# Kernel optimization log

Hardware: AMD Instinct MI355X
Metric: run time of the kernel (lower is better)

The kernel has to match this reference:

```python
import jax, jax.numpy as jnp
import numpy as np
import math

WH, WW = 8, 8
N = WH * WW            # tokens per window = 64
DIM = 128
H = 4                  # num_heads
HD = DIM // H          # head_dim = 32
B_ = 3072              # num_windows * batch
NW = 192               # windows per image (96/8 * 128/8)
LAMBDA_INIT = 0.8 - 0.6 * math.exp(-0.3 * 0)  # layer_idx = 0 -> 0.2
EPS_RMS = 1e-9


def _polar_input():
    # Polar-coordinate relative positions, as in __init__
    gy, gx = jnp.meshgrid(jnp.arange(WH), jnp.arange(WW), indexing='ij')
    flat = jnp.stack([gy.reshape(-1), gx.reshape(-1)])          # (2, N)
    rel = flat[:, :, None] - flat[:, None, :]                   # (2, N, N)
    dx = rel[1].astype(jnp.float32)
    dy = -rel[0].astype(jnp.float32)
    r = jnp.sqrt(dx * dx + dy * dy + 1e-9)
    theta = jnp.arctan2(dx, dy)
    max_r = math.sqrt((WH - 1) ** 2 + (WW - 1) ** 2)
    return jnp.stack([r / max_r, (theta + math.pi) / (2 * math.pi)], axis=-1)  # (N, N, 2)


def setup_inputs() -> dict:
    key = jax.random.key(0)
    ks = jax.random.split(key, 16)
    s = 0.02
    inp = {}
    inp['x'] = jax.random.normal(ks[0], (B_, N, DIM), jnp.float32)
    inp['mask'] = jnp.zeros((NW, N, N), jnp.float32)
    inp['Wqkv'] = jax.random.normal(ks[1], (3 * DIM, DIM), jnp.float32) * s
    inp['bqkv'] = jnp.zeros((3 * DIM,), jnp.float32)
    inp['Wqkv2'] = jax.random.normal(ks[2], (2 * DIM, DIM), jnp.float32) * s
    inp['bqkv2'] = jnp.zeros((2 * DIM,), jnp.float32)
    inp['Wp1'] = jax.random.normal(ks[3], (64, 2), jnp.float32) * 0.1
    inp['bp1'] = jnp.zeros((64,), jnp.float32)
    inp['Wp2'] = jax.random.normal(ks[4], (H, 64), jnp.float32) * 0.1
    inp['bp2'] = jnp.zeros((H,), jnp.float32)
    inp['lambda_q1'] = jax.random.normal(ks[5], (HD // 2,), jnp.float32) * 0.1
    inp['lambda_k1'] = jax.random.normal(ks[6], (HD // 2,), jnp.float32) * 0.1
    inp['lambda_q2'] = jax.random.normal(ks[7], (HD // 2,), jnp.float32) * 0.1
    inp['lambda_k2'] = jax.random.normal(ks[8], (HD // 2,), jnp.float32) * 0.1
    inp['subln_w'] = jnp.ones((HD,), jnp.float32)
    inp['Wproj'] = jax.random.normal(ks[9], (DIM, DIM), jnp.float32) * s
    inp['bproj'] = jnp.zeros((DIM,), jnp.float32)
    return inp


def reference(x, mask, Wqkv, bqkv, Wqkv2, bqkv2, Wp1, bp1, Wp2, bp2,
              lambda_q1, lambda_k1, lambda_q2, lambda_k2, subln_w, Wproj, bproj):
    scale = HD ** -0.5
    # primary q, k, v
    qkv = (x @ Wqkv.T + bqkv).reshape(B_, N, 3, H, HD).transpose(2, 0, 3, 1, 4)
    q, k, v = qkv[0] * scale, qkv[1], qkv[2]        # (B_, H, N, HD)
    # secondary q2, k2 for differential attention
    qk2 = (x @ Wqkv2.T + bqkv2).reshape(B_, N, 2, H, HD).transpose(2, 0, 3, 1, 4)
    q2, k2 = qk2[0] * scale, qk2[1]

    attn = jnp.einsum('bhnd,bhmd->bhnm', q, k)      # (B_, H, N, N)
    attn2 = jnp.einsum('bhnd,bhmd->bhnm', q2, k2)

    lam = (jnp.exp(jnp.sum(lambda_q1 * lambda_k1))
           - jnp.exp(jnp.sum(lambda_q2 * lambda_k2)) + LAMBDA_INIT)

    # MLP-based polar relative position bias (exact erf GELU, as nn.GELU)
    pin = _polar_input().reshape(-1, 2)
    pb = jax.nn.gelu(pin @ Wp1.T + bp1, approximate=False) @ Wp2.T + bp2
    pb = pb.reshape(N, N, H).transpose(2, 0, 1)     # (H, N, N)

    attn = attn - lam * attn2 + pb[None]
    # window mask (0 / -inf), broadcast over batch and heads
    attn = attn.reshape(B_ // NW, NW, H, N, N) + mask[None, :, None]
    attn = jax.nn.softmax(attn.reshape(B_, H, N, N), axis=-1)

    o = jnp.einsum('bhnm,bhmd->bhnd', attn, v)      # (B_, H, N, HD)
    # post-attention RMSNorm over head_dim, then differential rescale
    o = o * jax.lax.rsqrt(jnp.mean(o * o, axis=-1, keepdims=True) + EPS_RMS) * subln_w
    o = (o * (1.0 - LAMBDA_INIT)).transpose(0, 2, 1, 3).reshape(B_, N, DIM)
    return o @ Wproj.T + bproj
```

## Files before the change

kernel.cpp:

```cpp
#include <hip/hip_runtime.h>
#include <math.h>

typedef __attribute__((ext_vector_type(8))) short bf16x8;
typedef __attribute__((ext_vector_type(4))) float f32x4;

#define NWMASK 192
#define SCALE_Q 0.17677669529663687f

__device__ __forceinline__ unsigned short f2bf(float f) {
  union { float f; unsigned u; } v; v.f = f;
  return (unsigned short)((v.u + 0x7fffu + ((v.u >> 16) & 1u)) >> 16);
}

__device__ __forceinline__ bf16x8 pack8(const float* src) {
  float4 lo = *(const float4*)(src);
  float4 hi = *(const float4*)(src + 4);
  bf16x8 pk;
  pk[0] = (short)f2bf(lo.x); pk[1] = (short)f2bf(lo.y);
  pk[2] = (short)f2bf(lo.z); pk[3] = (short)f2bf(lo.w);
  pk[4] = (short)f2bf(hi.x); pk[5] = (short)f2bf(hi.y);
  pk[6] = (short)f2bf(hi.z); pk[7] = (short)f2bf(hi.w);
  return pk;
}

__global__ void wpack_kernel(const float* __restrict__ Wqkv, const float* __restrict__ Wqkv2,
                             const float* __restrict__ Wproj, unsigned short* __restrict__ Wb) {
  int gid = blockIdx.x * 256 + threadIdx.x;
  if (gid >= 12288) return;
  int l15 = gid & 15, quad = (gid >> 4) & 3, ks = (gid >> 6) & 3, ft = gid >> 8;
  int row = ft * 16 + l15;
  const float* src = (row < 384) ? (Wqkv + (size_t)row * 128)
                   : (row < 640) ? (Wqkv2 + (size_t)(row - 384) * 128)
                                 : (Wproj + (size_t)(row - 640) * 128);
  *(bf16x8*)(Wb + (size_t)gid * 8) = pack8(src + ks * 32 + quad * 8);
}

__global__ void pbt_kernel(const float* __restrict__ Wp1, const float* __restrict__ bp1,
                           const float* __restrict__ Wp2, const float* __restrict__ bp2,
                           float* __restrict__ pbT) {
  int idx = blockIdx.x * 256 + threadIdx.x;
  if (idx >= 4096) return;
  int i = idx >> 6, j = idx & 63;
  float dx = (float)((i & 7) - (j & 7));
  float dy = -(float)((i >> 3) - (j >> 3));
  float r = sqrtf(dx*dx + dy*dy + 1e-9f);
  float theta = atan2f(dx, dy);
  float p0 = r * (1.0f / 9.899494936611665f);
  float p1 = (theta + 3.14159265358979323846f) * (1.0f / 6.283185307179586f);
  float a0 = 0.f, a1 = 0.f, a2 = 0.f, a3 = 0.f;
  for (int f = 0; f < 64; ++f) {
    float hpre = p0 * Wp1[2*f] + p1 * Wp1[2*f+1] + bp1[f];
    float g = 0.5f * hpre * (1.0f + erff(hpre * 0.70710678118654752f));
    a0 += Wp2[f]       * g;
    a1 += Wp2[64 + f]  * g;
    a2 += Wp2[128 + f] * g;
    a3 += Wp2[192 + f] * g;
  }
  int o = j * 64 + i;
  pbT[o]          = a0 + bp2[0];
  pbT[4096 + o]   = a1 + bp2[1];
  pbT[8192 + o]   = a2 + bp2[2];
  pbT[12288 + o]  = a3 + bp2[3];
}

__global__ void maskt_kernel(const float* __restrict__ mask, float* __restrict__ maskT) {
  int gid = blockIdx.x * 256 + threadIdx.x;
  if (gid >= 786432) return;
  int wm = gid >> 12, rc = gid & 4095, c = rc >> 6, r = rc & 63;
  maskT[gid] = mask[(size_t)wm * 4096 + r * 64 + c];
}

__global__ __launch_bounds__(256, 2)
void fused_win(const float* __restrict__ x, const unsigned short* __restrict__ Wb,
               const float* __restrict__ bqkv, const float* __restrict__ bqkv2,
               const float* __restrict__ lq1, const float* __restrict__ lk1,
               const float* __restrict__ lq2, const float* __restrict__ lk2,
               const float* __restrict__ subln, const float* __restrict__ bproj,
               const float* __restrict__ pbT, const float* __restrict__ maskT,
               float* __restrict__ out) {
  __shared__ unsigned short smem[32768];

  const int b = blockIdx.x;
  const int t = threadIdx.x;
  const int w = t >> 6;
  const int lane = t & 63;
  const int l15 = lane & 15;
  const int quad = lane >> 4;
  const int h = w;
  const f32x4 zero4 = (f32x4){0.f, 0.f, 0.f, 0.f};

  {
    const float* xg = x + (size_t)b * 8192;
#pragma unroll
    for (int u = 0; u < 4; ++u) {
      int id = u * 256 + t;
      int r = id >> 4, c16 = id & 15;
      *(bf16x8*)(&smem[r * 128 + ((c16 ^ (r & 7)) * 8)]) = pack8(xg + r * 128 + c16 * 8);
    }
  }
  __syncthreads();

  float lam;
  {
    float s1 = 0.f, s2 = 0.f;
#pragma unroll
    for (int i = 0; i < 16; ++i) { s1 += lq1[i]*lk1[i]; s2 += lq2[i]*lk2[i]; }
    lam = expf(s1) - expf(s2) + 0.2f;
  }

  unsigned short* SW = smem + 8192 + w * 6144;

  auto ldXB = [&](int mi, int ks) -> bf16x8 {
    int row = mi * 16 + l15;
    return *(const bf16x8*)(&smem[row * 128 + (((ks * 4 + quad) ^ (l15 & 7)) * 8)]);
  };
  auto ldWbF = [&](int ft, int ks) -> bf16x8 {
    return *(const bf16x8*)(Wb + ((((size_t)ft * 4 + ks) * 4 + quad) * 16 + l15) * 8);
  };

  auto proj4 = [&](int ft0, int ft1, int ft2, int ft3, f32x4 acc[4][4]) {
#pragma unroll
    for (int mi = 0; mi < 4; ++mi)
#pragma unroll
      for (int nj = 0; nj < 4; ++nj) acc[mi][nj] = zero4;
#pragma unroll
    for (int ks = 0; ks < 4; ++ks) {
      bf16x8 xa[4], wf[4];
#pragma unroll
      for (int mi = 0; mi < 4; ++mi) xa[mi] = ldXB(mi, ks);
      wf[0] = ldWbF(ft0, ks); wf[1] = ldWbF(ft1, ks);
      wf[2] = ldWbF(ft2, ks); wf[3] = ldWbF(ft3, ks);
#pragma unroll
      for (int mi = 0; mi < 4; ++mi)
#pragma unroll
        for (int nj = 0; nj < 4; ++nj)
          acc[mi][nj] = __builtin_amdgcn_mfma_f32_16x16x32_bf16(xa[mi], wf[nj], acc[mi][nj], 0, 0, 0);
    }
  };
  auto storeQK = [&](f32x4 acc[4][4], const float* biasA, const float* biasB, float scA) {
#pragma unroll
    for (int nj = 0; nj < 4; ++nj) {
      int c32 = (nj & 1) * 16 + l15;
      float bias = (nj < 2) ? biasA[c32] : biasB[c32];
      float sc = (nj < 2) ? scA : 1.0f;
      unsigned short* buf = SW + ((nj < 2) ? 0 : 2048);
#pragma unroll
      for (int mi = 0; mi < 4; ++mi)
#pragma unroll
        for (int reg = 0; reg < 4; ++reg) {
          int row = mi * 16 + quad * 4 + reg;
          buf[row * 32 + (((c32 >> 3) ^ (row & 3)) * 8) + (c32 & 7)] =
              f2bf((acc[mi][nj][reg] + bias) * sc);
        }
    }
  };
  auto qkTiles = [&](f32x4 S[4][4], bool withBias) {
    bf16x8 qa[4], kb[4];
#pragma unroll
    for (int mi = 0; mi < 4; ++mi) {
      int row = mi * 16 + l15;
      qa[mi] = *(const bf16x8*)(&SW[row * 32 + ((quad ^ (l15 & 3)) * 8)]);
      kb[mi] = *(const bf16x8*)(&SW[2048 + row * 32 + ((quad ^ (l15 & 3)) * 8)]);
    }
    const float* pbh = pbT + h * 4096;
    const float* mkh = maskT + (size_t)(b % NWMASK) * 4096;
#pragma unroll
    for (int mi = 0; mi < 4; ++mi)
#pragma unroll
      for (int ni = 0; ni < 4; ++ni) {
        f32x4 c;
        if (withBias) {
          int off = (ni * 16 + l15) * 64 + mi * 16 + quad * 4;
          float4 p4 = *(const float4*)(pbh + off);
          float4 m4 = *(const float4*)(mkh + off);
          c[0] = p4.x + m4.x; c[1] = p4.y + m4.y;
          c[2] = p4.z + m4.z; c[3] = p4.w + m4.w;
        } else c = zero4;
        S[mi][ni] = __builtin_amdgcn_mfma_f32_16x16x32_bf16(qa[mi], kb[ni], c, 0, 0, 0);
      }
  };

  f32x4 S2[4][4];
  {
    f32x4 acc[4][4];
    proj4(24 + 2*h, 25 + 2*h, 32 + 2*h, 33 + 2*h, acc);
    storeQK(acc, bqkv2 + h*32, bqkv2 + 128 + h*32, SCALE_Q);
    qkTiles(S2, false);
  }
  f32x4 S[4][4];
  {
    f32x4 acc[4][4];
    proj4(2*h, 1 + 2*h, 8 + 2*h, 9 + 2*h, acc);
    storeQK(acc, bqkv + h*32, bqkv + 128 + h*32, SCALE_Q);
    qkTiles(S, true);
#pragma unroll
    for (int mi = 0; mi < 4; ++mi)
#pragma unroll
      for (int ni = 0; ni < 4; ++ni)
#pragma unroll
        for (int reg = 0; reg < 4; ++reg)
          S[mi][ni][reg] -= lam * S2[mi][ni][reg];
  }

#pragma unroll
  for (int mi = 0; mi < 4; ++mi) {
#pragma unroll
    for (int reg = 0; reg < 4; ++reg) {
      float mx = fmaxf(fmaxf(S[mi][0][reg], S[mi][1][reg]),
                       fmaxf(S[mi][2][reg], S[mi][3][reg]));
      mx = fmaxf(mx, __shfl_xor(mx, 1));
      mx = fmaxf(mx, __shfl_xor(mx, 2));
      mx = fmaxf(mx, __shfl_xor(mx, 4));
      mx = fmaxf(mx, __shfl_xor(mx, 8));
      float e0 = __expf(S[mi][0][reg] - mx);
      float e1 = __expf(S[mi][1][reg] - mx);
      float e2 = __expf(S[mi][2][reg] - mx);
      float e3 = __expf(S[mi][3][reg] - mx);
      float sum = e0 + e1 + e2 + e3;
      sum += __shfl_xor(sum, 1);
      sum += __shfl_xor(sum, 2);
      sum += __shfl_xor(sum, 4);
      sum += __shfl_xor(sum, 8);
      float inv = 1.0f / sum;
      int row = mi * 16 + quad * 4 + reg;
      int sw = row & 7;
      unsigned short* prow = SW + row * 64;
      prow[(((l15 >> 3) + 0) ^ sw) * 8 + (l15 & 7)] = f2bf(e0 * inv);
      prow[(((l15 >> 3) + 2) ^ sw) * 8 + (l15 & 7)] = f2bf(e1 * inv);
      prow[(((l15 >> 3) + 4) ^ sw) * 8 + (l15 & 7)] = f2bf(e2 * inv);
      prow[(((l15 >> 3) + 6) ^ sw) * 8 + (l15 & 7)] = f2bf(e3 * inv);
    }
  }

  {
    f32x4 av[4][2];
#pragma unroll
    for (int mi = 0; mi < 4; ++mi) { av[mi][0] = zero4; av[mi][1] = zero4; }
#pragma unroll
    for (int ks = 0; ks < 4; ++ks) {
      bf16x8 xa[4];
#pragma unroll
      for (int mi = 0; mi < 4; ++mi) xa[mi] = ldXB(mi, ks);
      bf16x8 w0 = ldWbF(16 + 2*h, ks), w1 = ldWbF(17 + 2*h, ks);
#pragma unroll
      for (int mi = 0; mi < 4; ++mi) {
        av[mi][0] = __builtin_amdgcn_mfma_f32_16x16x32_bf16(xa[mi], w0, av[mi][0], 0, 0, 0);
        av[mi][1] = __builtin_amdgcn_mfma_f32_16x16x32_bf16(xa[mi], w1, av[mi][1], 0, 0, 0);
      }
    }
#pragma unroll
    for (int nd = 0; nd < 2; ++nd) {
      int d = nd * 16 + l15;
      float bias = bqkv[256 + h * 32 + d];
#pragma unroll
      for (int mi = 0; mi < 4; ++mi) {
        int tok0 = mi * 16 + quad * 4;
        ushort4 pk;
        pk.x = f2bf(av[mi][nd][0] + bias);
        pk.y = f2bf(av[mi][nd][1] + bias);
        pk.z = f2bf(av[mi][nd][2] + bias);
        pk.w = f2bf(av[mi][nd][3] + bias);
        *(ushort4*)(&SW[4096 + d * 64 + (((tok0 >> 3) ^ (d & 7)) * 8) + (tok0 & 7)]) = pk;
      }
    }
  }

  float ov0[4][4], ov1[4][4];
  {
    f32x4 O[4][2];
#pragma unroll
    for (int mi = 0; mi < 4; ++mi) { O[mi][0] = zero4; O[mi][1] = zero4; }
#pragma unroll
    for (int kc = 0; kc < 2; ++kc) {
      bf16x8 pa[4], vb[2];
#pragma unroll
      for (int mi = 0; mi < 4; ++mi) {
        int row = mi * 16 + l15;
        pa[mi] = *(const bf16x8*)(&SW[row * 64 + (((kc * 4 + quad) ^ (l15 & 7)) * 8)]);
      }
#pragma unroll
      for (int nd = 0; nd < 2; ++nd) {
        int d = nd * 16 + l15;
        vb[nd] = *(const bf16x8*)(&SW[4096 + d * 64 + (((kc * 4 + quad) ^ (d & 7)) * 8)]);
      }
#pragma unroll
      for (int mi = 0; mi < 4; ++mi) {
        O[mi][0] = __builtin_amdgcn_mfma_f32_16x16x32_bf16(pa[mi], vb[0], O[mi][0], 0, 0, 0);
        O[mi][1] = __builtin_amdgcn_mfma_f32_16x16x32_bf16(pa[mi], vb[1], O[mi][1], 0, 0, 0);
      }
    }
    float sw0 = subln[l15] * 0.8f;
    float sw1 = subln[16 + l15] * 0.8f;
#pragma unroll
    for (int mi = 0; mi < 4; ++mi)
#pragma unroll
      for (int reg = 0; reg < 4; ++reg) {
        float a0 = O[mi][0][reg], a1 = O[mi][1][reg];
        float ss = a0 * a0 + a1 * a1;
        ss += __shfl_xor(ss, 1);
        ss += __shfl_xor(ss, 2);
        ss += __shfl_xor(ss, 4);
        ss += __shfl_xor(ss, 8);
        float rs = 1.0f / sqrtf(ss * (1.0f / 32.0f) + 1e-9f);
        ov0[mi][reg] = a0 * rs * sw0;
        ov1[mi][reg] = a1 * rs * sw1;
      }
  }

  __syncthreads();

  {
    int c0 = h * 32 + l15, c1 = h * 32 + 16 + l15;
#pragma unroll
    for (int mi = 0; mi < 4; ++mi)
#pragma unroll
      for (int reg = 0; reg < 4; ++reg) {
        int row = mi * 16 + quad * 4 + reg;
        unsigned short* orow = smem + 8192 + row * 128;
        orow[(((c0 >> 3) ^ (row & 7)) * 8) + (c0 & 7)] = f2bf(ov0[mi][reg]);
        orow[(((c1 >> 3) ^ (row & 7)) * 8) + (c1 & 7)] = f2bf(ov1[mi][reg]);
      }
  }
  __syncthreads();

  {
    f32x4 po[4][2];
#pragma unroll
    for (int mi = 0; mi < 4; ++mi) { po[mi][0] = zero4; po[mi][1] = zero4; }
#pragma unroll
    for (int ks = 0; ks < 4; ++ks) {
      bf16x8 oa[4];
#pragma unroll
      for (int mi = 0; mi < 4; ++mi) {
        int row = mi * 16 + l15;
        oa[mi] = *(const bf16x8*)(&smem[8192 + row * 128 + (((ks * 4 + quad) ^ (l15 & 7)) * 8)]);
      }
      bf16x8 w0 = ldWbF(40 + 2*w, ks), w1 = ldWbF(41 + 2*w, ks);
#pragma unroll
      for (int mi = 0; mi < 4; ++mi) {
        po[mi][0] = __builtin_amdgcn_mfma_f32_16x16x32_bf16(oa[mi], w0, po[mi][0], 0, 0, 0);
        po[mi][1] = __builtin_amdgcn_mfma_f32_16x16x32_bf16(oa[mi], w1, po[mi][1], 0, 0, 0);
      }
    }
    float* og = out + (size_t)b * 8192;
#pragma unroll
    for (int nt = 0; nt < 2; ++nt) {
      int col = (2 * w + nt) * 16 + l15;
      float bp = bproj[col];
#pragma unroll
      for (int mi = 0; mi < 4; ++mi)
#pragma unroll
        for (int reg = 0; reg < 4; ++reg)
          og[(size_t)(mi * 16 + quad * 4 + reg) * 128 + col] = po[mi][nt][reg] + bp;
    }
  }
}

extern "C" void kernel_launch(void* const* d_in, const int* in_sizes, int n_in,
                              void* d_out, int out_size, void* d_ws, size_t ws_size,
                              hipStream_t stream) {
  (void)in_sizes; (void)n_in; (void)out_size; (void)ws_size;
  const float* x     = (const float*)d_in[0];
  const float* mask  = (const float*)d_in[1];
  const float* Wqkv  = (const float*)d_in[2];
  const float* bqkv  = (const float*)d_in[3];
  const float* Wqkv2 = (const float*)d_in[4];
  const float* bqkv2 = (const float*)d_in[5];
  const float* Wp1   = (const float*)d_in[6];
  const float* bp1   = (const float*)d_in[7];
  const float* Wp2   = (const float*)d_in[8];
  const float* bp2   = (const float*)d_in[9];
  const float* lq1   = (const float*)d_in[10];
  const float* lk1   = (const float*)d_in[11];
  const float* lq2   = (const float*)d_in[12];
  const float* lk2   = (const float*)d_in[13];
  const float* subln = (const float*)d_in[14];
  const float* Wproj = (const float*)d_in[15];
  const float* bproj = (const float*)d_in[16];
  float* out = (float*)d_out;

  unsigned short* Wb = (unsigned short*)d_ws;
  float* pbT   = (float*)((char*)d_ws + 262144);
  float* maskT = (float*)((char*)d_ws + 327680);

  hipLaunchKernelGGL(wpack_kernel, dim3(48), dim3(256), 0, stream, Wqkv, Wqkv2, Wproj, Wb);
  hipLaunchKernelGGL(pbt_kernel, dim3(16), dim3(256), 0, stream, Wp1, bp1, Wp2, bp2, pbT);
  hipLaunchKernelGGL(maskt_kernel, dim3(3072), dim3(256), 0, stream, mask, maskT);
  hipLaunchKernelGGL(fused_win, dim3(3072), dim3(256), 0, stream,
                     x, Wb, bqkv, bqkv2, lq1, lk1, lq2, lk2, subln, bproj,
                     pbT, maskT, out);
}
```

Baseline: 324.3 us.

## Shrink LDS footprint by reusing x buffer for V, raise occupancy to three blocks

Measured after the change: 312.8 us. 1.04x faster.

```diff
diff --git a/kernel.cpp b/kernel.cpp
--- a/kernel.cpp
+++ b/kernel.cpp
@@ -12,15 +12,26 @@
   return (unsigned short)((v.u + 0x7fffu + ((v.u >> 16) & 1u)) >> 16);
 }
 
-__device__ __forceinline__ bf16x8 pack8(const float* src) {
+__device__ __forceinline__ unsigned pkbf(float a, float b) {
+#if defined(__has_builtin)
+#if __has_builtin(__builtin_amdgcn_cvt_pk_bf16_f32)
+  auto r = __builtin_amdgcn_cvt_pk_bf16_f32(a, b);
+  union { decltype(r) v; unsigned u; } c; c.v = r; return c.u;
+#else
+  return (unsigned)f2bf(a) | ((unsigned)f2bf(b) << 16);
+#endif
+#else
+  return (unsigned)f2bf(a) | ((unsigned)f2bf(b) << 16);
+#endif
+}
+
+__device__ __forceinline__ void pack8s(unsigned short* dst, const float* src) {
   float4 lo = *(const float4*)(src);
   float4 hi = *(const float4*)(src + 4);
-  bf16x8 pk;
-  pk[0] = (short)f2bf(lo.x); pk[1] = (short)f2bf(lo.y);
-  pk[2] = (short)f2bf(lo.z); pk[3] = (short)f2bf(lo.w);
-  pk[4] = (short)f2bf(hi.x); pk[5] = (short)f2bf(hi.y);
-  pk[6] = (short)f2bf(hi.z); pk[7] = (short)f2bf(hi.w);
-  return pk;
+  uint4 pk;
+  pk.x = pkbf(lo.x, lo.y); pk.y = pkbf(lo.z, lo.w);
+  pk.z = pkbf(hi.x, hi.y); pk.w = pkbf(hi.z, hi.w);
+  *(uint4*)dst = pk;
 }
 
 __global__ void wpack_kernel(const float* __restrict__ Wqkv, const float* __restrict__ Wqkv2,
@@ -32,7 +43,7 @@
   const float* src = (row < 384) ? (Wqkv + (size_t)row * 128)
                    : (row < 640) ? (Wqkv2 + (size_t)(row - 384) * 128)
                                  : (Wproj + (size_t)(row - 640) * 128);
-  *(bf16x8*)(Wb + (size_t)gid * 8) = pack8(src + ks * 32 + quad * 8);
+  pack8s(Wb + (size_t)gid * 8, src + ks * 32 + quad * 8);
 }
 
 __global__ void pbt_kernel(const float* __restrict__ Wp1, const float* __restrict__ bp1,
@@ -70,7 +81,7 @@
   maskT[gid] = mask[(size_t)wm * 4096 + r * 64 + c];
 }
 
-__global__ __launch_bounds__(256, 2)
+__global__ __launch_bounds__(256, 3)
 void fused_win(const float* __restrict__ x, const unsigned short* __restrict__ Wb,
                const float* __restrict__ bqkv, const float* __restrict__ bqkv2,
                const float* __restrict__ lq1, const float* __restrict__ lk1,
@@ -78,7 +89,7 @@
                const float* __restrict__ subln, const float* __restrict__ bproj,
                const float* __restrict__ pbT, const float* __restrict__ maskT,
                float* __restrict__ out) {
-  __shared__ unsigned short smem[32768];
+  __shared__ unsigned short smem[24576];
 
   const int b = blockIdx.x;
   const int t = threadIdx.x;
@@ -95,7 +106,7 @@
     for (int u = 0; u < 4; ++u) {
       int id = u * 256 + t;
       int r = id >> 4, c16 = id & 15;
-      *(bf16x8*)(&smem[r * 128 + ((c16 ^ (r & 7)) * 8)]) = pack8(xg + r * 128 + c16 * 8);
+      pack8s(&smem[r * 128 + ((c16 ^ (r & 7)) * 8)], xg + r * 128 + c16 * 8);
     }
   }
   __syncthreads();
@@ -108,7 +119,7 @@
     lam = expf(s1) - expf(s2) + 0.2f;
   }
 
-  unsigned short* SW = smem + 8192 + w * 6144;
+  unsigned short* PW = smem + 8192 + w * 4096;
 
   auto ldXB = [&](int mi, int ks) -> bf16x8 {
     int row = mi * 16 + l15;
@@ -143,15 +154,17 @@
       int c32 = (nj & 1) * 16 + l15;
       float bias = (nj < 2) ? biasA[c32] : biasB[c32];
       float sc = (nj < 2) ? scA : 1.0f;
-      unsigned short* buf = SW + ((nj < 2) ? 0 : 2048);
-#pragma unroll
-      for (int mi = 0; mi < 4; ++mi)
-#pragma unroll
-        for (int reg = 0; reg < 4; ++reg) {
-          int row = mi * 16 + quad * 4 + reg;
-          buf[row * 32 + (((c32 >> 3) ^ (row & 3)) * 8) + (c32 & 7)] =
-              f2bf((acc[mi][nj][reg] + bias) * sc);
-        }
+      unsigned short* buf = PW + ((nj < 2) ? 0 : 2048);
+#pragma unroll
+      for (int mi = 0; mi < 4; ++mi) {
+        unsigned p01 = pkbf((acc[mi][nj][0] + bias) * sc, (acc[mi][nj][1] + bias) * sc);
+        unsigned p23 = pkbf((acc[mi][nj][2] + bias) * sc, (acc[mi][nj][3] + bias) * sc);
+        int r0 = mi * 16 + quad * 4;
+        buf[(r0+0) * 32 + (((c32 >> 3) ^ ((r0+0) & 3)) * 8) + (c32 & 7)] = (unsigned short)p01;
+        buf[(r0+1) * 32 + (((c32 >> 3) ^ ((r0+1) & 3)) * 8) + (c32 & 7)] = (unsigned short)(p01 >> 16);
+        buf[(r0+2) * 32 + (((c32 >> 3) ^ ((r0+2) & 3)) * 8) + (c32 & 7)] = (unsigned short)p23;
+        buf[(r0+3) * 32 + (((c32 >> 3) ^ ((r0+3) & 3)) * 8) + (c32 & 7)] = (unsigned short)(p23 >> 16);
+      }
     }
   };
   auto qkTiles = [&](f32x4 S[4][4], bool withBias) {
@@ -159,8 +172,8 @@
 #pragma unroll
     for (int mi = 0; mi < 4; ++mi) {
       int row = mi * 16 + l15;
-      qa[mi] = *(const bf16x8*)(&SW[row * 32 + ((quad ^ (l15 & 3)) * 8)]);
-      kb[mi] = *(const bf16x8*)(&SW[2048 + row * 32 + ((quad ^ (l15 & 3)) * 8)]);
+      qa[mi] = *(const bf16x8*)(&PW[row * 32 + ((quad ^ (l15 & 3)) * 8)]);
+      kb[mi] = *(const bf16x8*)(&PW[2048 + row * 32 + ((quad ^ (l15 & 3)) * 8)]);
     }
     const float* pbh = pbT + h * 4096;
     const float* mkh = maskT + (size_t)(b % NWMASK) * 4096;
@@ -224,16 +237,18 @@
       float inv = 1.0f / sum;
       int row = mi * 16 + quad * 4 + reg;
       int sw = row & 7;
-      unsigned short* prow = SW + row * 64;
-      prow[(((l15 >> 3) + 0) ^ sw) * 8 + (l15 & 7)] = f2bf(e0 * inv);
-      prow[(((l15 >> 3) + 2) ^ sw) * 8 + (l15 & 7)] = f2bf(e1 * inv);
-      prow[(((l15 >> 3) + 4) ^ sw) * 8 + (l15 & 7)] = f2bf(e2 * inv);
-      prow[(((l15 >> 3) + 6) ^ sw) * 8 + (l15 & 7)] = f2bf(e3 * inv);
-    }
-  }
-
-  {
-    f32x4 av[4][2];
+      unsigned short* prow = PW + row * 64;
+      unsigned p01 = pkbf(e0 * inv, e1 * inv);
+      unsigned p23 = pkbf(e2 * inv, e3 * inv);
+      prow[(((l15 >> 3) + 0) ^ sw) * 8 + (l15 & 7)] = (unsigned short)p01;
+      prow[(((l15 >> 3) + 2) ^ sw) * 8 + (l15 & 7)] = (unsigned short)(p01 >> 16);
+      prow[(((l15 >> 3) + 4) ^ sw) * 8 + (l15 & 7)] = (unsigned short)p23;
+      prow[(((l15 >> 3) + 6) ^ sw) * 8 + (l15 & 7)] = (unsigned short)(p23 >> 16);
+    }
+  }
+
+  f32x4 av[4][2];
+  {
 #pragma unroll
     for (int mi = 0; mi < 4; ++mi) { av[mi][0] = zero4; av[mi][1] = zero4; }
 #pragma unroll
@@ -248,6 +263,11 @@
         av[mi][1] = __builtin_amdgcn_mfma_f32_16x16x32_bf16(xa[mi], w1, av[mi][1], 0, 0, 0);
       }
     }
+  }
+  __syncthreads();
+
+  {
+    unsigned short* VT = smem + w * 2048;
 #pragma unroll
     for (int nd = 0; nd < 2; ++nd) {
       int d = nd * 16 + l15;
@@ -255,18 +275,17 @@
 #pragma unroll
       for (int mi = 0; mi < 4; ++mi) {
         int tok0 = mi * 16 + quad * 4;
-        ushort4 pk;
-        pk.x = f2bf(av[mi][nd][0] + bias);
-        pk.y = f2bf(av[mi][nd][1] + bias);
-        pk.z = f2bf(av[mi][nd][2] + bias);
-        pk.w = f2bf(av[mi][nd][3] + bias);
-        *(ushort4*)(&SW[4096 + d * 64 + (((tok0 >> 3) ^ (d & 7)) * 8) + (tok0 & 7)]) = pk;
+        uint2 pk;
+        pk.x = pkbf(av[mi][nd][0] + bias, av[mi][nd][1] + bias);
+        pk.y = pkbf(av[mi][nd][2] + bias, av[mi][nd][3] + bias);
+        *(uint2*)(&VT[d * 64 + (((tok0 >> 3) ^ (d & 7)) * 8) + (tok0 & 7)]) = pk;
       }
     }
   }
 
   float ov0[4][4], ov1[4][4];
   {
+    unsigned short* VT = smem + w * 2048;
     f32x4 O[4][2];
 #pragma unroll
     for (int mi = 0; mi < 4; ++mi) { O[mi][0] = zero4; O[mi][1] = zero4; }
@@ -276,12 +295,12 @@
 #pragma unroll
       for (int mi = 0; mi < 4; ++mi) {
         int row = mi * 16 + l15;
-        pa[mi] = *(const bf16x8*)(&SW[row * 64 + (((kc * 4 + quad) ^ (l15 & 7)) * 8)]);
+        pa[mi] = *(const bf16x8*)(&PW[row * 64 + (((kc * 4 + quad) ^ (row & 7)) * 8)]);
       }
 #pragma unroll
       for (int nd = 0; nd < 2; ++nd) {
         int d = nd * 16 + l15;
-        vb[nd] = *(const bf16x8*)(&SW[4096 + d * 64 + (((kc * 4 + quad) ^ (d & 7)) * 8)]);
+        vb[nd] = *(const bf16x8*)(&VT[d * 64 + (((kc * 4 + quad) ^ (d & 7)) * 8)]);
       }
 #pragma unroll
       for (int mi = 0; mi < 4; ++mi) {
@@ -317,8 +336,9 @@
       for (int reg = 0; reg < 4; ++reg) {
         int row = mi * 16 + quad * 4 + reg;
         unsigned short* orow = smem + 8192 + row * 128;
-        orow[(((c0 >> 3) ^ (row & 7)) * 8) + (c0 & 7)] = f2bf(ov0[mi][reg]);
-        orow[(((c1 >> 3) ^ (row & 7)) * 8) + (c1 & 7)] = f2bf(ov1[mi][reg]);
+        unsigned p = pkbf(ov0[mi][reg], ov1[mi][reg]);
+        orow[(((c0 >> 3) ^ (row & 7)) * 8) + (c0 & 7)] = (unsigned short)p;
+        orow[(((c1 >> 3) ^ (row & 7)) * 8) + (c1 & 7)] = (unsigned short)(p >> 16);
       }
   }
   __syncthreads();
```
